# Optimization experiments

Measured on AMD Instinct MI355X. Metric: run time of the kernel, lower is better.

## Reference

```python
import jax, jax.numpy as jnp
import numpy as np

B, L, D, N = 4, 4096, 1024, 1024  # d_state must equal d_model for the original broadcasting to work


def _bayes_linear(x, wmu, wlv, bmu, blv, key):
    """Reparameterized Bayesian linear: w = mu + exp(0.5*log_var)*eps."""
    kw, kb = jax.random.split(key)
    w = wmu + jnp.exp(0.5 * wlv) * jax.random.normal(kw, wmu.shape, wmu.dtype)
    b = bmu + jnp.exp(0.5 * blv) * jax.random.normal(kb, bmu.shape, bmu.dtype)
    return x @ w.T + b


def setup_inputs() -> dict:
    key = jax.random.key(0)
    ks = jax.random.split(key, 17)
    inp = {"x": jax.random.normal(ks[0], (B, L, D), jnp.float32)}
    shapes = {"A": (N, D), "Bp": (N, D), "C": (D, N), "dt": (N, D)}
    i = 1
    for name, (o, ii) in shapes.items():
        # torch init: mu ~ N(0, 0.1), log_var ~ N(-9, 0.1)
        inp[f"{name}_wmu"] = 0.1 * jax.random.normal(ks[i], (o, ii), jnp.float32); i += 1
        inp[f"{name}_wlv"] = -9.0 + 0.1 * jax.random.normal(ks[i], (o, ii), jnp.float32); i += 1
        inp[f"{name}_bmu"] = 0.1 * jax.random.normal(ks[i], (o,), jnp.float32); i += 1
        inp[f"{name}_blv"] = -9.0 + 0.1 * jax.random.normal(ks[i], (o,), jnp.float32); i += 1
    return inp


def reference(x, A_wmu, A_wlv, A_bmu, A_blv,
              Bp_wmu, Bp_wlv, Bp_bmu, Bp_blv,
              C_wmu, C_wlv, C_bmu, C_blv,
              dt_wmu, dt_wlv, dt_bmu, dt_blv):
    key = jax.random.key(42)
    kA, kB, kC, kdt = jax.random.split(key, 4)
    A = -jnp.exp(_bayes_linear(x, A_wmu, A_wlv, A_bmu, A_blv, kA))   # [B,L,N]
    dt = jnp.exp(_bayes_linear(x, dt_wmu, dt_wlv, dt_bmu, dt_blv, kdt))
    Bm = _bayes_linear(x, Bp_wmu, Bp_wlv, Bp_bmu, Bp_blv, kB)        # [B,L,N]
    C = _bayes_linear(x, C_wmu, C_wlv, C_bmu, C_blv, kC)             # [B,L,D]

    E = jnp.exp(A * dt)   # per-step decay, [B,L,N]
    Bx = Bm * x           # input injection (requires N == D, as in original)

    def step(h, inp):
        e, bx, c = inp
        h = h * e + bx
        return h, c * h

    ET = jnp.swapaxes(E, 0, 1)    # time-major [L,B,N]
    BxT = jnp.swapaxes(Bx, 0, 1)
    CT = jnp.swapaxes(C, 0, 1)
    h0 = jnp.zeros((x.shape[0], N), x.dtype)
    _, yT = jax.lax.scan(step, h0, (ET, BxT, CT))
    # The torch code broadcasts h to [B,B,N] and sums over dim=1; h is identical
    # along that axis, so the sum equals multiplying by batch_size.
    return jnp.swapaxes(yT, 0, 1) * x.shape[0]
```

## Files before the change

### kernel.cpp

```cpp
#include <hip/hip_runtime.h>
#include <cstdint>

__host__ __device__ inline void tf2x32(uint32_t k0, uint32_t k1,
                                       uint32_t x0, uint32_t x1,
                                       uint32_t& o0, uint32_t& o1) {
  uint32_t ks2 = k0 ^ k1 ^ 0x1BD11BDAu;
  uint32_t v0 = x0 + k0, v1 = x1 + k1;
#define TFR(r) { v0 += v1; v1 = (v1 << r) | (v1 >> (32 - r)); v1 ^= v0; }
  TFR(13) TFR(15) TFR(26) TFR(6)
  v0 += k1;  v1 += ks2 + 1u;
  TFR(17) TFR(29) TFR(16) TFR(24)
  v0 += ks2; v1 += k0 + 2u;
  TFR(13) TFR(15) TFR(26) TFR(6)
  v0 += k0;  v1 += k1 + 3u;
  TFR(17) TFR(29) TFR(16) TFR(24)
  v0 += k1;  v1 += ks2 + 4u;
  TFR(13) TFR(15) TFR(26) TFR(6)
  v0 += ks2; v1 += k0 + 5u;
#undef TFR
  o0 = v0; o1 = v1;
}

__device__ inline float erfinv32(float x) {
  float w = -log1pf(-x * x);
  float p;
  if (w < 5.0f) {
    w -= 2.5f;
    p = 2.81022636e-08f;
    p = fmaf(p, w, 3.43273939e-07f);
    p = fmaf(p, w, -3.5233877e-06f);
    p = fmaf(p, w, -4.39150654e-06f);
    p = fmaf(p, w, 0.00021858087f);
    p = fmaf(p, w, -0.00125372503f);
    p = fmaf(p, w, -0.00417768164f);
    p = fmaf(p, w, 0.246640727f);
    p = fmaf(p, w, 1.50140941f);
  } else {
    w = sqrtf(w) - 3.0f;
    p = -0.000200214257f;
    p = fmaf(p, w, 0.000100950558f);
    p = fmaf(p, w, 0.00134934322f);
    p = fmaf(p, w, -0.00367342844f);
    p = fmaf(p, w, 0.00573950773f);
    p = fmaf(p, w, -0.0076224613f);
    p = fmaf(p, w, 0.00943887047f);
    p = fmaf(p, w, 1.00167406f);
    p = fmaf(p, w, 2.83297682f);
  }
  return p * x;
}

__device__ inline float rng_normal(uint32_t k0, uint32_t k1, uint32_t idx) {
  uint32_t o0, o1;
  tf2x32(k0, k1, 0u, idx, o0, o1);
  uint32_t bits = o0 ^ o1;
  float f = __uint_as_float((bits >> 9) | 0x3f800000u) - 1.0f;
  const float lo = -0.999999940395355224609375f;
  float u = fmaxf(lo, f * 2.0f + lo);
  return 1.41421356237f * erfinv32(u);
}

struct RngKeys {
  uint32_t wA0, wA1, bA0, bA1;
  uint32_t wB0, wB1, bB0, bB1;
  uint32_t wC0, wC1, bC0, bC1;
  uint32_t wD0, wD1, bD0, bD1;
};

typedef _Float16 f16x8 __attribute__((ext_vector_type(8)));
typedef _Float16 f16x4 __attribute__((ext_vector_type(4)));
typedef float f32x4 __attribute__((ext_vector_type(4)));

__global__ __launch_bounds__(256) void gen_weights(
    const float* __restrict__ Awmu, const float* __restrict__ Awlv,
    const float* __restrict__ Dwmu, const float* __restrict__ Dwlv,
    const float* __restrict__ Bwmu, const float* __restrict__ Bwlv,
    const float* __restrict__ Cwmu, const float* __restrict__ Cwlv,
    _Float16* __restrict__ Wh, RngKeys kk) {
  uint32_t idx = blockIdx.x * 256u + threadIdx.x;
  uint32_t sel = idx >> 20;
  uint32_t e = idx & 0xFFFFFu;
  float w;
  if (sel == 0u) {
    w = Awmu[e] + expf(0.5f * Awlv[e]) * rng_normal(kk.wA0, kk.wA1, e)
      + Dwmu[e] + expf(0.5f * Dwlv[e]) * rng_normal(kk.wD0, kk.wD1, e);
  } else if (sel == 1u) {
    w = Bwmu[e] + expf(0.5f * Bwlv[e]) * rng_normal(kk.wB0, kk.wB1, e);
  } else {
    w = Cwmu[e] + expf(0.5f * Cwlv[e]) * rng_normal(kk.wC0, kk.wC1, e);
  }
  Wh[idx] = (_Float16)w;
}

__global__ __launch_bounds__(256) void gen_bias(
    const float* __restrict__ Abmu, const float* __restrict__ Ablv,
    const float* __restrict__ Dbmu, const float* __restrict__ Dblv,
    const float* __restrict__ Bbmu, const float* __restrict__ Bblv,
    const float* __restrict__ Cbmu, const float* __restrict__ Cblv,
    float* __restrict__ bcat, RngKeys kk) {
  uint32_t o = blockIdx.x * 256u + threadIdx.x;
  uint32_t e = o & 1023u;
  float b;
  if (o < 1024u)
    b = Abmu[e] + expf(0.5f * Ablv[e]) * rng_normal(kk.bA0, kk.bA1, e)
      + Dbmu[e] + expf(0.5f * Dblv[e]) * rng_normal(kk.bD0, kk.bD1, e);
  else if (o < 2048u)
    b = Bbmu[e] + expf(0.5f * Bblv[e]) * rng_normal(kk.bB0, kk.bB1, e);
  else
    b = Cbmu[e] + expf(0.5f * Cblv[e]) * rng_normal(kk.bC0, kk.bC1, e);
  bcat[o] = b;
}

__global__ __launch_bounds__(256) void convert_x(const float* __restrict__ X,
                                                 _Float16* __restrict__ Xh) {
  size_t i4 = ((size_t)blockIdx.x * 256 + threadIdx.x) * 4;
  float4 v = *(const float4*)(X + i4);
  f16x4 h;
  h[0] = (_Float16)v.x; h[1] = (_Float16)v.y;
  h[2] = (_Float16)v.z; h[3] = (_Float16)v.w;
  *(f16x4*)(Xh + i4) = h;
}

__device__ inline void gl2lds16(const void* g, void* l) {
  __builtin_amdgcn_global_load_lds(
      (const __attribute__((address_space(1))) void*)g,
      (__attribute__((address_space(3))) void*)l, 16, 0, 0);
}

#define STAGE_U(BUF, KT, KC)                                   \
  do {                                                         \
    const _Float16* ga_ = gA + (KT) * 64 + (KC) * 32;          \
    const _Float16* gb_ = gB + (KT) * 64 + (KC) * 32;          \
    char* la_ = (char*)(&sA[(BUF)][(KC)][0]) + tid * 16;       \
    char* lb_ = (char*)(&sB[(BUF)][(KC)][0]) + tid * 16;       \
    gl2lds16(ga_, la_);                                        \
    gl2lds16(ga_ + 128 * 1024, la_ + 8192);                    \
    gl2lds16(gb_, lb_);                                        \
    gl2lds16(gb_ + 128 * 1024, lb_ + 8192);                    \
  } while (0)

#define HALF_TILE(CUR, KC)                                                    \
  do {                                                                        \
    _Pragma("unroll") for (int mf_ = 0; mf_ < 8; ++mf_)                       \
      ah[mf_] =                                                               \
          *(const f16x8*)&sA[(CUR)][(KC)][(abase + mf_ * 16) * 32 + qo];      \
    _Pragma("unroll") for (int nf_ = 0; nf_ < 4; ++nf_)                       \
      bh[nf_] =                                                               \
          *(const f16x8*)&sB[(CUR)][(KC)][(bbase + nf_ * 16) * 32 + qo];      \
    asm volatile("s_waitcnt lgkmcnt(0)" ::: "memory");                        \
    __builtin_amdgcn_sched_barrier(0);                                        \
    __builtin_amdgcn_s_setprio(1);                                            \
    _Pragma("unroll") for (int mf_ = 0; mf_ < 8; ++mf_)                       \
      _Pragma("unroll") for (int nf_ = 0; nf_ < 4; ++nf_)                     \
        acc[mf_][nf_] = __builtin_amdgcn_mfma_f32_16x16x32_f16(               \
            ah[mf_], bh[nf_], acc[mf_][nf_], 0, 0, 0);                        \
    __builtin_amdgcn_s_setprio(0);                                            \
  } while (0)

__global__ __launch_bounds__(512, 2) void gemm_fused(
    const _Float16* __restrict__ Xh, const _Float16* __restrict__ Wh,
    const float* __restrict__ X, const float* __restrict__ bcat,
    _Float16* __restrict__ Z, float* __restrict__ out) {
  __shared__ _Float16 sA[2][2][256 * 32];
  __shared__ _Float16 sB[2][2][256 * 32];

  const int tid = threadIdx.x;

  const int swz = ((int)blockIdx.x & 7) * 96 + ((int)blockIdx.x >> 3);
  const int mt = swz / 12;
  const int nt = swz - mt * 12;
  const int m0 = mt * 256;
  const int n0 = nt * 256;

  const _Float16* gA = Xh + (size_t)(m0 + (tid >> 2)) * 1024 + (tid & 3) * 8;
  const _Float16* gB = Wh + (size_t)(n0 + (tid >> 2)) * 1024 + (tid & 3) * 8;

  const int lane = tid & 63;
  const int wave = tid >> 6;
  const int wm = wave >> 2;
  const int wn = wave & 3;
  const int fr = lane & 15;
  const int qo = (lane >> 4) * 8;

  const int abase = wm * 128 + fr;
  const int bbase = wn * 64 + fr;

  f32x4 acc[8][4] = {};
  f16x8 ah[8], bh[4];

  STAGE_U(0, 0, 0);
  STAGE_U(0, 0, 1);

  for (int kt = 0; kt < 15; ++kt) {
    const int cur = kt & 1;
    const int nxt = cur ^ 1;
    STAGE_U(nxt, kt + 1, 0);
    asm volatile("s_waitcnt vmcnt(8)" ::: "memory");
    __builtin_amdgcn_s_barrier();
    HALF_TILE(cur, 0);
    STAGE_U(nxt, kt + 1, 1);
    asm volatile("s_waitcnt vmcnt(8)" ::: "memory");
    __builtin_amdgcn_s_barrier();
    HALF_TILE(cur, 1);
    __builtin_amdgcn_s_barrier();
  }
  asm volatile("s_waitcnt vmcnt(4)" ::: "memory");
  __builtin_amdgcn_s_barrier();
  HALF_TILE(1, 0);
  asm volatile("s_waitcnt vmcnt(0)" ::: "memory");
  __builtin_amdgcn_s_barrier();
  HALF_TILE(1, 1);
  __builtin_amdgcn_sched_barrier(0);

  const int seg = n0 >> 10;
  const int mrow = (lane >> 4) * 4;
  const int mb0 = m0 + wm * 128;
#pragma unroll
  for (int nf = 0; nf < 4; ++nf) {
    const int n = n0 + wn * 64 + nf * 16 + fr;
    const float bv = bcat[n];
#pragma unroll
    for (int mf = 0; mf < 8; ++mf) {
      const int mbase = mb0 + mf * 16 + mrow;
      f32x4 a = acc[mf][nf];
#pragma unroll
      for (int r = 0; r < 4; ++r) {
        const int m = mbase + r;
        const float v = a[r] + bv;
        if (seg == 0) {
          Z[(size_t)m * 2048 + n] = (_Float16)expf(-expf(v));
        } else if (seg == 1) {
          Z[(size_t)m * 2048 + n] =
              (_Float16)(v * X[(size_t)m * 1024 + (n - 1024)]);
        } else {
          out[(size_t)m * 1024 + (n - 2048)] = v;
        }
      }
    }
  }
}

#define LSEQ 4096
#define NC 64
#define LC 64
#define ZW 2048

__global__ __launch_bounds__(256) void scan_chunk(const _Float16* __restrict__ Z,
                                                  float* __restrict__ ac,
                                                  float* __restrict__ uc) {
  int n = blockIdx.x * 256 + threadIdx.x;
  int c = blockIdx.y;
  int b = blockIdx.z;
  const _Float16* base = Z + (size_t)(b * LSEQ + c * LC) * ZW;
  float a = 1.0f, u = 0.0f;
#pragma unroll 4
  for (int l = 0; l < LC; ++l) {
    float e  = (float)base[(size_t)l * ZW + n];
    float bx = (float)base[(size_t)l * ZW + 1024 + n];
    a *= e;
    u = fmaf(e, u, bx);
  }
  size_t o = ((size_t)b * NC + c) * 1024 + n;
  ac[o] = a;
  uc[o] = u;
}

__global__ __launch_bounds__(256) void scan_prefix(const float* __restrict__ ac,
                                                   const float* __restrict__ uc,
                                                   float* __restrict__ hin) {
  int idx = blockIdx.x * 256 + threadIdx.x;
  int b = idx >> 10, n = idx & 1023;
  float h = 0.0f;
  for (int c = 0; c < NC; ++c) {
    size_t o = ((size_t)b * NC + c) * 1024 + n;
    hin[o] = h;
    h = fmaf(ac[o], h, uc[o]);
  }
}

__global__ __launch_bounds__(256) void scan_final(const _Float16* __restrict__ Z,
                                                  const float* __restrict__ hin,
                                                  float* __restrict__ out) {
  int n = blockIdx.x * 256 + threadIdx.x;
  int c = blockIdx.y;
  int b = blockIdx.z;
  const _Float16* base = Z + (size_t)(b * LSEQ + c * LC) * ZW;
  float* obase = out + (size_t)(b * LSEQ + c * LC) * 1024;
  float h = hin[((size_t)b * NC + c) * 1024 + n];
#pragma unroll 4
  for (int l = 0; l < LC; ++l) {
    float e  = (float)base[(size_t)l * ZW + n];
    float bx = (float)base[(size_t)l * ZW + 1024 + n];
    float cc = obase[(size_t)l * 1024 + n];
    h = fmaf(e, h, bx);
    obase[(size_t)l * 1024 + n] = cc * h * 4.0f;
  }
}

extern "C" void kernel_launch(void* const* d_in, const int* in_sizes, int n_in,
                              void* d_out, int out_size, void* d_ws, size_t ws_size,
                              hipStream_t stream) {
  const float* x    = (const float*)d_in[0];
  const float* Awmu = (const float*)d_in[1];
  const float* Awlv = (const float*)d_in[2];
  const float* Abmu = (const float*)d_in[3];
  const float* Ablv = (const float*)d_in[4];
  const float* Bwmu = (const float*)d_in[5];
  const float* Bwlv = (const float*)d_in[6];
  const float* Bbmu = (const float*)d_in[7];
  const float* Bblv = (const float*)d_in[8];
  const float* Cwmu = (const float*)d_in[9];
  const float* Cwlv = (const float*)d_in[10];
  const float* Cbmu = (const float*)d_in[11];
  const float* Cblv = (const float*)d_in[12];
  const float* Dwmu = (const float*)d_in[13];
  const float* Dwlv = (const float*)d_in[14];
  const float* Dbmu = (const float*)d_in[15];
  const float* Dblv = (const float*)d_in[16];

  uint32_t k4[4][2];
  for (uint32_t i = 0; i < 4; ++i)
    tf2x32(0u, 42u, 0u, i, k4[i][0], k4[i][1]);
  RngKeys kk;
  tf2x32(k4[0][0], k4[0][1], 0u, 0u, kk.wA0, kk.wA1);
  tf2x32(k4[0][0], k4[0][1], 0u, 1u, kk.bA0, kk.bA1);
  tf2x32(k4[1][0], k4[1][1], 0u, 0u, kk.wB0, kk.wB1);
  tf2x32(k4[1][0], k4[1][1], 0u, 1u, kk.bB0, kk.bB1);
  tf2x32(k4[2][0], k4[2][1], 0u, 0u, kk.wC0, kk.wC1);
  tf2x32(k4[2][0], k4[2][1], 0u, 1u, kk.bC0, kk.bC1);
  tf2x32(k4[3][0], k4[3][1], 0u, 0u, kk.wD0, kk.wD1);
  tf2x32(k4[3][0], k4[3][1], 0u, 1u, kk.bD0, kk.bD1);

  char* ws = (char*)d_ws;
  const size_t OFF_WH   = 0;
  const size_t OFF_BCAT = 6291456;
  const size_t OFF_XH   = 8388608;
  const size_t OFF_Z    = 41943040;
  const size_t OFF_AC   = OFF_Z + (size_t)16384 * 2048 * 2;
  const size_t OFF_UC   = OFF_AC + (size_t)4 * NC * 1024 * 4;
  const size_t OFF_HIN  = OFF_UC + (size_t)4 * NC * 1024 * 4;
  const size_t NEEDED   = OFF_HIN + (size_t)4 * NC * 1024 * 4;
  if (ws_size < NEEDED) return;

  _Float16* Wh  = (_Float16*)(ws + OFF_WH);
  float*    bcat= (float*)(ws + OFF_BCAT);
  _Float16* Xh  = (_Float16*)(ws + OFF_XH);
  _Float16* Z   = (_Float16*)(ws + OFF_Z);
  float*    ac  = (float*)(ws + OFF_AC);
  float*    ucv = (float*)(ws + OFF_UC);
  float*    hin = (float*)(ws + OFF_HIN);
  float*    out = (float*)d_out;

  gen_weights<<<dim3(12288), dim3(256), 0, stream>>>(
      Awmu, Awlv, Dwmu, Dwlv, Bwmu, Bwlv, Cwmu, Cwlv, Wh, kk);
  gen_bias<<<dim3(12), dim3(256), 0, stream>>>(
      Abmu, Ablv, Dbmu, Dblv, Bbmu, Bblv, Cbmu, Cblv, bcat, kk);
  convert_x<<<dim3(16384), dim3(256), 0, stream>>>(x, Xh);
  gemm_fused<<<dim3(768), dim3(512), 0, stream>>>(
      Xh, Wh, x, bcat, Z, out);
  scan_chunk<<<dim3(4, NC, 4), dim3(256), 0, stream>>>(Z, ac, ucv);
  scan_prefix<<<dim3(16), dim3(256), 0, stream>>>(ac, ucv, hin);
  scan_final<<<dim3(4, NC, 4), dim3(256), 0, stream>>>(Z, hin, out);
}
```

Measured before the change: 433.1 us.

## Restructure GEMM into swizzled quadrant pipeline and vectorize scan kernels

The GEMM main loop now stages 128x64 half-tiles with an XOR-swizzled LDS layout, which is meant to cut bank conflicts. It computes the 256x256 tile as four quadrants, interleaving the LDS reads, the next-tile global loads and the MFMAs to overlap them better. The scan_chunk and scan_final kernels now process 4 channels per thread with vector loads and stores, on a grid four times smaller. The smaller scan grid (256 blocks) may underfill the GPU, and the new quadrant schedule adds barriers and register pressure.

```diff
diff --git a/kernel.cpp b/kernel.cpp
--- a/kernel.cpp
+++ b/kernel.cpp
@@ -127,42 +127,72 @@
       (__attribute__((address_space(3))) void*)l, 16, 0, 0);
 }
 
-#define STAGE_U(BUF, KT, KC)                                   \
-  do {                                                         \
-    const _Float16* ga_ = gA + (KT) * 64 + (KC) * 32;          \
-    const _Float16* gb_ = gB + (KT) * 64 + (KC) * 32;          \
-    char* la_ = (char*)(&sA[(BUF)][(KC)][0]) + tid * 16;       \
-    char* lb_ = (char*)(&sB[(BUF)][(KC)][0]) + tid * 16;       \
-    gl2lds16(ga_, la_);                                        \
-    gl2lds16(ga_ + 128 * 1024, la_ + 8192);                    \
-    gl2lds16(gb_, lb_);                                        \
-    gl2lds16(gb_ + 128 * 1024, lb_ + 8192);                    \
-  } while (0)
-
-#define HALF_TILE(CUR, KC)                                                    \
-  do {                                                                        \
-    _Pragma("unroll") for (int mf_ = 0; mf_ < 8; ++mf_)                       \
-      ah[mf_] =                                                               \
-          *(const f16x8*)&sA[(CUR)][(KC)][(abase + mf_ * 16) * 32 + qo];      \
-    _Pragma("unroll") for (int nf_ = 0; nf_ < 4; ++nf_)                       \
-      bh[nf_] =                                                               \
-          *(const f16x8*)&sB[(CUR)][(KC)][(bbase + nf_ * 16) * 32 + qo];      \
-    asm volatile("s_waitcnt lgkmcnt(0)" ::: "memory");                        \
-    __builtin_amdgcn_sched_barrier(0);                                        \
-    __builtin_amdgcn_s_setprio(1);                                            \
-    _Pragma("unroll") for (int mf_ = 0; mf_ < 8; ++mf_)                       \
-      _Pragma("unroll") for (int nf_ = 0; nf_ < 4; ++nf_)                     \
-        acc[mf_][nf_] = __builtin_amdgcn_mfma_f32_16x16x32_f16(               \
-            ah[mf_], bh[nf_], acc[mf_][nf_], 0, 0, 0);                        \
-    __builtin_amdgcn_s_setprio(0);                                            \
+#define STAGE_A(BUF, KT, H)                                            \
+  do {                                                                 \
+    const _Float16* g_ = gA0 + (size_t)((H) * 128) * 1024 + (KT) * 64; \
+    char* l_ = (char*)(&sA[(BUF)][(H)][0]) + tid * 16;                 \
+    gl2lds16(g_, l_);                                                  \
+    gl2lds16(g_ + 64 * 1024, l_ + 8192);                               \
+  } while (0)
+
+#define STAGE_B(BUF, KT, H)                                            \
+  do {                                                                 \
+    const _Float16* g_ = gB0 + (size_t)((H) * 128) * 1024 + (KT) * 64; \
+    char* l_ = (char*)(&sB[(BUF)][(H)][0]) + tid * 16;                 \
+    gl2lds16(g_, l_);                                                  \
+    gl2lds16(g_ + 64 * 1024, l_ + 8192);                               \
+  } while (0)
+
+#define READ_A(CUR, MH)                                                \
+  do {                                                                 \
+    _Pragma("unroll") for (int k_ = 0; k_ < 4; ++k_) {                 \
+      const int ro_ = abase + k_ * 1024;                               \
+      ah[2 * k_]     = *(const f16x8*)&sA[(CUR)][(MH)][ro_ + so0];     \
+      ah[2 * k_ + 1] = *(const f16x8*)&sA[(CUR)][(MH)][ro_ + so1];     \
+    }                                                                  \
+  } while (0)
+
+#define READ_B(CUR, NH)                                                \
+  do {                                                                 \
+    _Pragma("unroll") for (int j_ = 0; j_ < 2; ++j_) {                 \
+      const int ro_ = bbase + j_ * 1024;                               \
+      bh[2 * j_]     = *(const f16x8*)&sB[(CUR)][(NH)][ro_ + so0];     \
+      bh[2 * j_ + 1] = *(const f16x8*)&sB[(CUR)][(NH)][ro_ + so1];     \
+    }                                                                  \
+  } while (0)
+
+#define QUAD(MH, NH)                                                         \
+  do {                                                                       \
+    _Pragma("unroll") for (int k_ = 0; k_ < 4; ++k_)                         \
+      _Pragma("unroll") for (int j_ = 0; j_ < 2; ++j_) {                     \
+        f32x4 c_ = acc[(MH) * 4 + k_][(NH) * 2 + j_];                        \
+        c_ = __builtin_amdgcn_mfma_f32_16x16x32_f16(ah[2 * k_], bh[2 * j_],  \
+                                                    c_, 0, 0, 0);            \
+        c_ = __builtin_amdgcn_mfma_f32_16x16x32_f16(                         \
+            ah[2 * k_ + 1], bh[2 * j_ + 1], c_, 0, 0, 0);                    \
+        acc[(MH) * 4 + k_][(NH) * 2 + j_] = c_;                              \
+      }                                                                      \
+  } while (0)
+
+#define VMW(N) asm volatile("s_waitcnt vmcnt(" #N ")" ::: "memory")
+#define MFMA_PRE()                                       \
+  do {                                                   \
+    asm volatile("s_waitcnt lgkmcnt(0)" ::: "memory");   \
+    __builtin_amdgcn_sched_barrier(0);                   \
+    __builtin_amdgcn_s_setprio(1);                       \
+  } while (0)
+#define MFMA_POST()                                      \
+  do {                                                   \
+    __builtin_amdgcn_s_setprio(0);                       \
+    __builtin_amdgcn_s_barrier();                        \
   } while (0)
 
 __global__ __launch_bounds__(512, 2) void gemm_fused(
     const _Float16* __restrict__ Xh, const _Float16* __restrict__ Wh,
     const float* __restrict__ X, const float* __restrict__ bcat,
     _Float16* __restrict__ Z, float* __restrict__ out) {
-  __shared__ _Float16 sA[2][2][256 * 32];
-  __shared__ _Float16 sB[2][2][256 * 32];
+  __shared__ _Float16 sA[2][2][128 * 64];
+  __shared__ _Float16 sB[2][2][128 * 64];
 
   const int tid = threadIdx.x;
 
@@ -172,57 +202,87 @@
   const int m0 = mt * 256;
   const int n0 = nt * 256;
 
-  const _Float16* gA = Xh + (size_t)(m0 + (tid >> 2)) * 1024 + (tid & 3) * 8;
-  const _Float16* gB = Wh + (size_t)(n0 + (tid >> 2)) * 1024 + (tid & 3) * 8;
+  const int srow = tid >> 3;
+  const int sc = (tid & 7) ^ (srow & 7);
+  const _Float16* gA0 = Xh + (size_t)(m0 + srow) * 1024 + sc * 8;
+  const _Float16* gB0 = Wh + (size_t)(n0 + srow) * 1024 + sc * 8;
 
   const int lane = tid & 63;
   const int wave = tid >> 6;
   const int wm = wave >> 2;
   const int wn = wave & 3;
   const int fr = lane & 15;
-  const int qo = (lane >> 4) * 8;
-
-  const int abase = wm * 128 + fr;
-  const int bbase = wn * 64 + fr;
+  const int q = lane >> 4;
+  const int f7 = fr & 7;
+  const int so0 = (q ^ f7) * 8;
+  const int so1 = so0 ^ 32;
+
+  const int abase = (wm * 64 + fr) * 64;
+  const int bbase = (wn * 32 + fr) * 64;
 
   f32x4 acc[8][4] = {};
   f16x8 ah[8], bh[4];
 
-  STAGE_U(0, 0, 0);
-  STAGE_U(0, 0, 1);
+  STAGE_A(0, 0, 0);
+  STAGE_B(0, 0, 0);
+  STAGE_B(0, 0, 1);
+  STAGE_A(0, 0, 1);
+  VMW(4);
+  __builtin_amdgcn_s_barrier();
 
   for (int kt = 0; kt < 15; ++kt) {
     const int cur = kt & 1;
     const int nxt = cur ^ 1;
-    STAGE_U(nxt, kt + 1, 0);
-    asm volatile("s_waitcnt vmcnt(8)" ::: "memory");
+    READ_A(cur, 0);
+    READ_B(cur, 0);
+    STAGE_A(nxt, kt + 1, 0);
+    VMW(4);
     __builtin_amdgcn_s_barrier();
-    HALF_TILE(cur, 0);
-    STAGE_U(nxt, kt + 1, 1);
-    asm volatile("s_waitcnt vmcnt(8)" ::: "memory");
+    MFMA_PRE(); QUAD(0, 0); MFMA_POST();
+    READ_B(cur, 1);
+    STAGE_B(nxt, kt + 1, 0);
+    VMW(4);
     __builtin_amdgcn_s_barrier();
-    HALF_TILE(cur, 1);
+    MFMA_PRE(); QUAD(0, 1); MFMA_POST();
+    READ_A(cur, 1);
+    STAGE_B(nxt, kt + 1, 1);
     __builtin_amdgcn_s_barrier();
-  }
-  asm volatile("s_waitcnt vmcnt(4)" ::: "memory");
+    MFMA_PRE(); QUAD(1, 1); MFMA_POST();
+    READ_B(cur, 0);
+    STAGE_A(nxt, kt + 1, 1);
+    VMW(4);
+    __builtin_amdgcn_s_barrier();
+    MFMA_PRE(); QUAD(1, 0); MFMA_POST();
+  }
+  READ_A(1, 0);
+  READ_B(1, 0);
+  VMW(2);
   __builtin_amdgcn_s_barrier();
-  HALF_TILE(1, 0);
-  asm volatile("s_waitcnt vmcnt(0)" ::: "memory");
+  MFMA_PRE(); QUAD(0, 0); MFMA_POST();
+  READ_B(1, 1);
+  VMW(0);
   __builtin_amdgcn_s_barrier();
-  HALF_TILE(1, 1);
+  MFMA_PRE(); QUAD(0, 1); MFMA_POST();
+  READ_A(1, 1);
+  MFMA_PRE(); QUAD(1, 1);
+  __builtin_amdgcn_s_setprio(0);
+  READ_B(1, 0);
+  MFMA_PRE(); QUAD(1, 0);
+  __builtin_amdgcn_s_setprio(0);
   __builtin_amdgcn_sched_barrier(0);
 
   const int seg = n0 >> 10;
   const int mrow = (lane >> 4) * 4;
-  const int mb0 = m0 + wm * 128;
 #pragma unroll
-  for (int nf = 0; nf < 4; ++nf) {
-    const int n = n0 + wn * 64 + nf * 16 + fr;
+  for (int nfg = 0; nfg < 4; ++nfg) {
+    const int nh = nfg >> 1, j = nfg & 1;
+    const int n = n0 + wn * 32 + nh * 128 + j * 16 + fr;
     const float bv = bcat[n];
 #pragma unroll
     for (int mf = 0; mf < 8; ++mf) {
-      const int mbase = mb0 + mf * 16 + mrow;
-      f32x4 a = acc[mf][nf];
+      const int mh = mf >> 2, k = mf & 3;
+      const int mbase = m0 + wm * 64 + mh * 128 + k * 16 + mrow;
+      f32x4 a = acc[mf][nfg];
 #pragma unroll
       for (int r = 0; r < 4; ++r) {
         const int m = mbase + r;
@@ -248,21 +308,26 @@
 __global__ __launch_bounds__(256) void scan_chunk(const _Float16* __restrict__ Z,
                                                   float* __restrict__ ac,
                                                   float* __restrict__ uc) {
-  int n = blockIdx.x * 256 + threadIdx.x;
+  int n4 = threadIdx.x * 4;
   int c = blockIdx.y;
   int b = blockIdx.z;
   const _Float16* base = Z + (size_t)(b * LSEQ + c * LC) * ZW;
-  float a = 1.0f, u = 0.0f;
+  float a[4] = {1.0f, 1.0f, 1.0f, 1.0f};
+  float u[4] = {0.0f, 0.0f, 0.0f, 0.0f};
 #pragma unroll 4
   for (int l = 0; l < LC; ++l) {
-    float e  = (float)base[(size_t)l * ZW + n];
-    float bx = (float)base[(size_t)l * ZW + 1024 + n];
-    a *= e;
-    u = fmaf(e, u, bx);
-  }
-  size_t o = ((size_t)b * NC + c) * 1024 + n;
-  ac[o] = a;
-  uc[o] = u;
+    f16x4 ev = *(const f16x4*)&base[(size_t)l * ZW + n4];
+    f16x4 bx = *(const f16x4*)&base[(size_t)l * ZW + 1024 + n4];
+#pragma unroll
+    for (int i = 0; i < 4; ++i) {
+      float e = (float)ev[i];
+      a[i] *= e;
+      u[i] = fmaf(e, u[i], (float)bx[i]);
+    }
+  }
+  size_t o = ((size_t)b * NC + c) * 1024 + n4;
+  *(float4*)&ac[o] = make_float4(a[0], a[1], a[2], a[3]);
+  *(float4*)&uc[o] = make_float4(u[0], u[1], u[2], u[3]);
 }
 
 __global__ __launch_bounds__(256) void scan_prefix(const float* __restrict__ ac,
@@ -281,19 +346,25 @@
 __global__ __launch_bounds__(256) void scan_final(const _Float16* __restrict__ Z,
                                                   const float* __restrict__ hin,
                                                   float* __restrict__ out) {
-  int n = blockIdx.x * 256 + threadIdx.x;
+  int n4 = threadIdx.x * 4;
   int c = blockIdx.y;
   int b = blockIdx.z;
   const _Float16* base = Z + (size_t)(b * LSEQ + c * LC) * ZW;
   float* obase = out + (size_t)(b * LSEQ + c * LC) * 1024;
-  float h = hin[((size_t)b * NC + c) * 1024 + n];
+  size_t ho = ((size_t)b * NC + c) * 1024 + n4;
+  float4 hv = *(const float4*)&hin[ho];
+  float h[4] = {hv.x, hv.y, hv.z, hv.w};
 #pragma unroll 4
   for (int l = 0; l < LC; ++l) {
-    float e  = (float)base[(size_t)l * ZW + n];
-    float bx = (float)base[(size_t)l * ZW + 1024 + n];
-    float cc = obase[(size_t)l * 1024 + n];
-    h = fmaf(e, h, bx);
-    obase[(size_t)l * 1024 + n] = cc * h * 4.0f;
+    f16x4 ev = *(const f16x4*)&base[(size_t)l * ZW + n4];
+    f16x4 bx = *(const f16x4*)&base[(size_t)l * ZW + 1024 + n4];
+    float4 cc = *(const float4*)&obase[(size_t)l * 1024 + n4];
+#pragma unroll
+    for (int i = 0; i < 4; ++i)
+      h[i] = fmaf((float)ev[i], h[i], (float)bx[i]);
+    *(float4*)&obase[(size_t)l * 1024 + n4] =
+        make_float4(cc.x * h[0] * 4.0f, cc.y * h[1] * 4.0f,
+                    cc.z * h[2] * 4.0f, cc.w * h[3] * 4.0f);
   }
 }
 
@@ -358,7 +429,7 @@
   convert_x<<<dim3(16384), dim3(256), 0, stream>>>(x, Xh);
   gemm_fused<<<dim3(768), dim3(512), 0, stream>>>(
       Xh, Wh, x, bcat, Z, out);
-  scan_chunk<<<dim3(4, NC, 4), dim3(256), 0, stream>>>(Z, ac, ucv);
+  scan_chunk<<<dim3(1, NC, 4), dim3(256), 0, stream>>>(Z, ac, ucv);
   scan_prefix<<<dim3(16), dim3(256), 0, stream>>>(ac, ucv, hin);
-  scan_final<<<dim3(4, NC, 4), dim3(256), 0, stream>>>(Z, hin, out);
-}
+  scan_final<<<dim3(1, NC, 4), dim3(256), 0, stream>>>(Z, hin, out);
+}
```

Result: faster. 406.5 us (-6.1%).
